# Kernel tuning notes

Hardware: AMD Instinct MI355X
Metric: run time of the kernel (lower is better)

Reference implementation:

```python
import jax, jax.numpy as jnp
import numpy as np

K = 5            # kernel_size per dim
KD = K ** 3      # 125 spline weight slots
DIM = 3
NUM_GRAPHS = 64
# (n_nodes, n_edges, c_in, c_mid, c_out) per pyramid level
LEVELS = [(20000, 320000, 1, 32, 64), (10000, 160000, 1, 64, 64),
          (5000, 80000, 1, 64, 64), (2500, 40000, 1, 64, 64), (1250, 20000, 1, 64, 64)]


def setup_inputs() -> dict:
    key = jax.random.key(0)
    inp = {}
    for i, (n, e, cin, c1, c2) in enumerate(LEVELS, start=1):
        ks = jax.random.split(jax.random.fold_in(key, i), 8)
        inp[f'x{i}'] = jax.random.normal(ks[0], (n, cin), jnp.float32)
        inp[f'pseudo{i}'] = jax.random.uniform(ks[1], (e, DIM), jnp.float32)  # in [0,1)
        inp[f'edge_index{i}'] = jax.random.randint(ks[2], (2, e), 0, n)
        inp[f'batch{i}'] = jnp.sort(jax.random.randint(ks[3], (n,), 0, NUM_GRAPHS))
        inp[f'W{i}a'] = 0.1 * jax.random.normal(ks[4], (KD, cin, c1), jnp.float32)
        inp[f'root{i}a'] = 0.1 * jax.random.normal(ks[5], (cin, c1), jnp.float32)
        inp[f'bias{i}a'] = jnp.zeros((c1,), jnp.float32)
        inp[f'W{i}b'] = 0.1 * jax.random.normal(ks[6], (KD, c1, c2), jnp.float32)
        inp[f'root{i}b'] = 0.1 * jax.random.normal(ks[7], (c1, c2), jnp.float32)
        inp[f'bias{i}b'] = jnp.zeros((c2,), jnp.float32)
    kf = jax.random.fold_in(key, 99)
    inp['fc_w'] = 0.05 * jax.random.normal(kf, (5 * 64, 10), jnp.float32)
    inp['fc_b'] = jnp.zeros((10,), jnp.float32)
    return inp


def _spline_conv(x, src, dst, pseudo, W, Wroot, bias):
    """Degree-1 open B-spline conv (torch_spline_conv), mean aggregation + root weight."""
    n, cin = x.shape
    v = pseudo * (K - 1)                       # [E,3], pseudo in [0,1)
    k0 = jnp.floor(v).astype(jnp.int32)        # lower knot index per dim
    frac = v - k0                              # fractional part per dim
    xs = x[src]                                # [E,cin] gather source feats
    # accumulate basis-weighted source features per (target node, kernel slot)
    acc = jnp.zeros((n, KD, cin), x.dtype)
    for bits in range(2 ** DIM):               # 8 corner combinations of linear spline
        w = jnp.ones((src.shape[0],), x.dtype)
        idx = jnp.zeros((src.shape[0],), jnp.int32)
        for d in range(DIM):
            b = (bits >> d) & 1
            w = w * (frac[:, d] if b else 1.0 - frac[:, d])
            idx = idx * K + (k0[:, d] + b)
        acc = acc.at[dst, idx].add(w[:, None] * xs)
    deg = jnp.zeros((n,), x.dtype).at[dst].add(1.0)
    out = jnp.einsum('nki,kio->no', acc, W) / jnp.maximum(deg, 1.0)[:, None]
    return out + x @ Wroot + bias


def _readout(f, batch):
    s = jax.ops.segment_sum(f, batch, num_segments=NUM_GRAPHS)
    cnt = jax.ops.segment_sum(jnp.ones((f.shape[0],), f.dtype), batch, num_segments=NUM_GRAPHS)
    return s / jnp.maximum(cnt, 1.0)[:, None]   # scatter_mean


def _level(x, ei, ps, bt, Wa, ra, ba, Wb, rb, bb):
    f = jax.nn.relu(_spline_conv(x, ei[0], ei[1], ps, Wa, ra, ba))
    f = jax.nn.relu(_spline_conv(f, ei[0], ei[1], ps, Wb, rb, bb))
    return _readout(f, bt)


def reference(x1, pseudo1, edge_index1, batch1, W1a, root1a, bias1a, W1b, root1b, bias1b,
              x2, pseudo2, edge_index2, batch2, W2a, root2a, bias2a, W2b, root2b, bias2b,
              x3, pseudo3, edge_index3, batch3, W3a, root3a, bias3a, W3b, root3b, bias3b,
              x4, pseudo4, edge_index4, batch4, W4a, root4a, bias4a, W4b, root4b, bias4b,
              x5, pseudo5, edge_index5, batch5, W5a, root5a, bias5a, W5b, root5b, bias5b,
              fc_w, fc_b):
    levels = [
        (x1, edge_index1, pseudo1, batch1, W1a, root1a, bias1a, W1b, root1b, bias1b),
        (x2, edge_index2, pseudo2, batch2, W2a, root2a, bias2a, W2b, root2b, bias2b),
        (x3, edge_index3, pseudo3, batch3, W3a, root3a, bias3a, W3b, root3b, bias3b),
        (x4, edge_index4, pseudo4, batch4, W4a, root4a, bias4a, W4b, root4b, bias4b),
        (x5, edge_index5, pseudo5, batch5, W5a, root5a, bias5a, W5b, root5b, bias5b),
    ]
    res = [_level(*lv) for lv in levels]
    h = jnp.concatenate(res, axis=1)            # [B,320]; eval mode -> dropout is identity
    logits = h @ fc_w + fc_b                    # [B,10]
    return jax.nn.log_softmax(logits, axis=1)
```

## Files before the change

### kernel.cpp

```cpp
#include <hip/hip_runtime.h>
#include <hip/hip_fp16.h>
#include <math.h>

#define NUM_GRAPHS 64

typedef unsigned short ushortT;
typedef __attribute__((ext_vector_type(8))) short bf16x8;
typedef __attribute__((ext_vector_type(4))) float f32x4;

constexpr int cN[5]       = {20000, 10000, 5000, 2500, 1250};
constexpr int cE[5]       = {320000, 160000, 80000, 40000, 20000};
constexpr int cNOFF[6]    = {0, 20000, 30000, 35000, 37500, 38750};
constexpr int cEOFF[6]    = {0, 320000, 480000, 560000, 600000, 620000};
constexpr int cEBLKOFF[6] = {0, 1250, 1875, 2188, 2345, 2424};
constexpr int cNBLKOFF[6] = {0, 79, 119, 139, 149, 154};
constexpr int cMT[5]      = {5064, 2564, 1314, 689, 377};
constexpr int cTILEOFF[6] = {0, 5064, 7628, 8942, 9631, 10008};
constexpr int cSEOFF[6]   = {0, 324096, 488192, 572288, 616384, 640512};
constexpr int cF1OFF[6]   = {0, 640000, 1280000, 1600000, 1760000, 1840000};
constexpr int cWOFF[6]    = {0, 32000, 96000, 160000, 224000, 288000};
constexpr int cABLK[6]    = {0, 1250, 1875, 2188, 2345, 2424};
constexpr int cRBOFF[5]   = {0, 256, 768, 1280, 1792};
constexpr int cWAOFF[6]   = {0, 512, 1536, 2560, 3584, 4608};
constexpr int cRGB[6]     = {0, 313, 470, 549, 589, 609};

struct P5f { const float* p[5]; };
struct P5i { const int* p[5]; };

__device__ __forceinline__ int lvl_e(int b) {
    return (b >= cEBLKOFF[4]) ? 4 : (b >= cEBLKOFF[3]) ? 3 : (b >= cEBLKOFF[2]) ? 2 : (b >= cEBLKOFF[1]) ? 1 : 0;
}
__device__ __forceinline__ int lvl_n(int b) {
    return (b >= cNBLKOFF[4]) ? 4 : (b >= cNBLKOFF[3]) ? 3 : (b >= cNBLKOFF[2]) ? 2 : (b >= cNBLKOFF[1]) ? 1 : 0;
}

__device__ __forceinline__ ushortT f2bf(float f) {
    union { float f; unsigned int u; } v; v.f = f;
    unsigned int r = (v.u + 0x7FFFu + ((v.u >> 16) & 1u)) >> 16;
    return (ushortT)r;
}
__device__ __forceinline__ float h2f_lo(unsigned int u) {
    return __half2float(__ushort_as_half((ushortT)(u & 0xFFFFu)));
}
__device__ __forceinline__ float h2f_hi(unsigned int u) {
    return __half2float(__ushort_as_half((ushortT)(u >> 16)));
}

__global__ void k_hist(P5f PS, P5i EI, int* __restrict__ dcnt, int* __restrict__ bb) {
    int b = blockIdx.x;
    int l = lvl_e(b);
    int lb = b - cEBLKOFF[l];
    int E = cE[l];
    __shared__ int h[64];
    int t = threadIdx.x;
    if (t < 64) h[t] = 0;
    __syncthreads();
    int e = lb * 256 + t;
    if (e < E) {
        atomicAdd(&dcnt[cNOFF[l] + EI.p[l][E + e]], 1);
        const float* ps = PS.p[l];
        int c = (int)floorf(ps[e * 3] * 4.f) * 16 + (int)floorf(ps[e * 3 + 1] * 4.f) * 4
              + (int)floorf(ps[e * 3 + 2] * 4.f);
        atomicAdd(&h[c], 1);
    }
    __syncthreads();
    if (t < 64) bb[(size_t)b * 64 + t] = h[t];
}

__global__ void k_cellscan(int* __restrict__ bb_all, int* __restrict__ csPad,
                           int* __restrict__ cellTot, int* __restrict__ cot_all) {
    int l = blockIdx.x;
    int c = threadIdx.x;
    int* bb = bb_all + (size_t)cEBLKOFF[l] * 64;
    int nblk = cEBLKOFF[l + 1] - cEBLKOFF[l];
    int run = 0;
    int b = 0;
    for (; b + 16 <= nblk; b += 16) {
        int v[16];
#pragma unroll
        for (int u = 0; u < 16; u++) v[u] = bb[(b + u) * 64 + c];
#pragma unroll
        for (int u = 0; u < 16; u++) { bb[(b + u) * 64 + c] = run; run += v[u]; }
    }
    for (; b < nblk; b++) { int v = bb[b * 64 + c]; bb[b * 64 + c] = run; run += v; }
    int tot = run;
    cellTot[l * 64 + c] = tot;
    int tiles = (tot + 63) >> 6;
    int x = tiles;
#pragma unroll
    for (int off = 1; off < 64; off <<= 1) { int y = __shfl_up(x, off, 64); if (c >= off) x += y; }
    int tileBase = x - tiles;
    csPad[l * 64 + c] = tileBase * 64;
    int* cot = cot_all + cTILEOFF[l];
    for (int i = 0; i < tiles; i++) cot[tileBase + i] = c;
    int nT = __shfl(x, 63, 64);
    int mt = cMT[l];
    for (int i = nT + c; i < mt; i += 64) cot[i] = -1;
}

__global__ void k_nscan1(const int* __restrict__ dcnt, int* __restrict__ dbase, int* __restrict__ bsum) {
    int b = blockIdx.x;
    int l = lvl_n(b);
    int lb = b - cNBLKOFF[l];
    int n = cN[l];
    __shared__ int sh[256];
    int t = threadIdx.x;
    int i = lb * 256 + t;
    int v = (i < n) ? dcnt[cNOFF[l] + i] : 0;
    sh[t] = v;
    __syncthreads();
    for (int off = 1; off < 256; off <<= 1) {
        int y = (t >= off) ? sh[t - off] : 0;
        __syncthreads();
        sh[t] += y;
        __syncthreads();
    }
    if (i < n) dbase[cNOFF[l] + i] = sh[t] - v;
    if (t == 255) bsum[b] = sh[255];
}

__global__ void k_nscan2(const int* __restrict__ bsum, int* __restrict__ boff) {
    int l = blockIdx.x;
    int o = cNBLKOFF[l];
    int nb = cNBLKOFF[l + 1] - o;
    int t = threadIdx.x;
    int v = (t < nb) ? bsum[o + t] : 0;
    int s = v;
#pragma unroll
    for (int off = 1; off < 64; off <<= 1) { int y = __shfl_up(s, off, 64); if (t >= off) s += y; }
    int tot = __shfl(s, 63, 64);
    if (t < nb) boff[o + t] = s - v;
    int t2 = t + 64;
    int v2 = (t2 < nb) ? bsum[o + t2] : 0;
    int s2 = v2;
#pragma unroll
    for (int off = 1; off < 64; off <<= 1) { int y = __shfl_up(s2, off, 64); if (t >= off) s2 += y; }
    if (t2 < nb) boff[o + t2] = tot + s2 - v2;
}

__global__ void k_scatter(P5f PS, P5i EI, const int* __restrict__ bb, const int* __restrict__ csPad,
                          const int* __restrict__ dbase, const int* __restrict__ boff,
                          int* __restrict__ rank,
                          int4* __restrict__ cbrec, int4* __restrict__ darec,
                          int* __restrict__ cpos) {
    int b = blockIdx.x;
    int l = lvl_e(b);
    int lb = b - cEBLKOFF[l];
    int E = cE[l];
    __shared__ int base[64];
    __shared__ int cnt[64];
    int t = threadIdx.x;
    if (t < 64) { base[t] = bb[(size_t)b * 64 + t] + csPad[l * 64 + t]; cnt[t] = 0; }
    __syncthreads();
    int e = lb * 256 + t;
    if (e >= E) return;
    const float* ps = PS.p[l];
    float v0 = ps[e * 3] * 4.f, v1 = ps[e * 3 + 1] * 4.f, v2 = ps[e * 3 + 2] * 4.f;
    float f0 = floorf(v0), f1v = floorf(v1), f2v = floorf(v2);
    int c = (int)f0 * 16 + (int)f1v * 4 + (int)f2v;
    int r = atomicAdd(&cnt[c], 1);
    int posc = base[c] + r;
    const int* ei = EI.p[l];
    int src = ei[e];
    int dst = ei[E + e];
    int posd = dbase[cNOFF[l] + dst] + boff[cNBLKOFF[l] + (dst >> 8)]
             + atomicAdd(&rank[cNOFF[l] + dst], 1);
    unsigned int fxfy = (unsigned int)__half_as_ushort(__float2half(v0 - f0))
                      | ((unsigned int)__half_as_ushort(__float2half(v1 - f1v)) << 16);
    unsigned int fzp  = (unsigned int)__half_as_ushort(__float2half(v2 - f2v));
    int4 rc;
    rc.x = src; rc.y = 0; rc.z = (int)fxfy; rc.w = (int)fzp;
    cbrec[cSEOFF[l] + posc] = rc;
    int4 rd;
    rd.x = src | (dst << 16); rd.y = c; rd.z = (int)fxfy; rd.w = (int)fzp;
    darec[cEOFF[l] + posd] = rd;
    cpos[cEOFF[l] + posd] = posc;
}

__global__ void k_wswz(P5f WB, P5f RootB, P5f WA,
                       uint4* __restrict__ hi4, uint4* __restrict__ rb, uint4* __restrict__ wa) {
    int idx = blockIdx.x * 256 + threadIdx.x;
    if (idx >= 294912) return;
    if (idx < 288000) {
        int l = (idx >= 224000) ? 4 : (idx >= 160000) ? 3 : (idx >= 96000) ? 2 : (idx >= 32000) ? 1 : 0;
        int local = idx - cWOFF[l];
        int T = l ? 2 : 1, C = l ? 64 : 32;
        int lane = local & 63;
        int blk = (local >> 6) & 3;
        int rest = local >> 8;
        int st = rest % T, s = rest / T;
        int q = lane >> 4, n = blk * 16 + (lane & 15);
        const float* W = WB.p[l];
        union { ushortT u[8]; uint4 v; } ph;
#pragma unroll
        for (int j = 0; j < 8; j++) {
            int k = st * 32 + q * 8 + j;
            ph.u[j] = f2bf(W[((size_t)s * C + k) * 64 + n]);
        }
        hi4[idx] = ph.v;
    } else if (idx < 290304) {
        int id2 = idx - 288000;
        int l = (id2 >= 1792) ? 4 : (id2 >= 1280) ? 3 : (id2 >= 768) ? 2 : (id2 >= 256) ? 1 : 0;
        int local = id2 - cRBOFF[l];
        int lane = local & 63;
        int w = (local >> 6) & 3;
        int st = local >> 8;
        int q = lane >> 4, n = w * 16 + (lane & 15);
        const float* R = RootB.p[l];
        union { ushortT u[8]; uint4 v; } ph;
#pragma unroll
        for (int j = 0; j < 8; j++) {
            int k = st * 32 + q * 8 + j;
            ph.u[j] = f2bf(R[k * 64 + n]);
        }
        rb[id2] = ph.v;
    } else {
        int id3 = idx - 290304;
        int l = (id3 >= cWAOFF[4]) ? 4 : (id3 >= cWAOFF[3]) ? 3 : (id3 >= cWAOFF[2]) ? 2 : (id3 >= cWAOFF[1]) ? 1 : 0;
        int local = id3 - cWAOFF[l];
        int C1 = l ? 64 : 32;
        int numN = C1 / 16;
        int lane = local & 63;
        int rest = local >> 6;
        int nb = rest % numN, st = rest / numN;
        int q = lane >> 4, n = nb * 16 + (lane & 15);
        const float* Wsrc = WA.p[l];
        union { ushortT u[8]; uint4 v; } ph;
#pragma unroll
        for (int j = 0; j < 8; j++) {
            int k = st * 32 + q * 8 + j;
            ph.u[j] = (k < 125) ? f2bf(Wsrc[k * C1 + n]) : (ushortT)0;
        }
        wa[id3] = ph.v;
    }
}

__launch_bounds__(256)
__global__ void conv_a_fused(P5f X, P5f RootA, P5f BiasA,
                             const int4* __restrict__ darec, const uint4* __restrict__ wasw,
                             const int* __restrict__ dbase, const int* __restrict__ boff,
                             const int* __restrict__ dcnt, ushortT* __restrict__ f1bf) {
    __shared__ float S[16 * 126];
    __shared__ ushortT Sbf[16 * 136];
    __shared__ int infoS[256];
    __shared__ unsigned int fxyS[256];
    __shared__ unsigned int fzS[256];
    __shared__ float xsS[256];
    int b = blockIdx.x;
    int l = (b >= cABLK[4]) ? 4 : (b >= cABLK[3]) ? 3 : (b >= cABLK[2]) ? 2 : (b >= cABLK[1]) ? 1 : 0;
    int node0 = (b - cABLK[l]) * 16;
    int n = cN[l];
    int nn = n - node0; if (nn > 16) nn = 16;
    int t = threadIdx.x;
    for (int i = t; i < 16 * 126; i += 256) S[i] = 0.f;
    const int* db = dbase + cNOFF[l];
    const int* bo = boff + cNBLKOFF[l];
    int estart = db[node0] + bo[node0 >> 8];
    int vend = node0 + nn;
    int eend = (vend >= n) ? cE[l] : (db[vend] + bo[vend >> 8]);
    const float* x = X.p[l];
    const int4* dr = darec + cEOFF[l];
    const int bx = t & 1, by = (t >> 1) & 1, bz = (t >> 2) & 1;
    for (int cs = estart; cs < eend; cs += 256) {
        int p = cs + t;
        if (p < eend) {
            int4 r = dr[p];
            infoS[t] = ((((unsigned int)r.x) >> 16) - node0) * 64 + r.y;
            fxyS[t] = (unsigned int)r.z;
            fzS[t] = (unsigned int)r.w;
            xsS[t] = x[r.x & 0xFFFF];
        }
        __syncthreads();
        int ne = eend - cs; if (ne > 256) ne = 256;
        for (int j = (t >> 3); j < ne; j += 32) {
            int info = infoS[j];
            int nl = info >> 6, cell = info & 63;
            unsigned int uz = fxyS[j];
            float fx = h2f_lo(uz), fy = h2f_hi(uz), fz = h2f_lo(fzS[j]);
            float xs = xsS[j];
            int cx = cell >> 4, cy = (cell >> 2) & 3, cz = cell & 3;
            int slot = (cx + bx) * 25 + (cy + by) * 5 + (cz + bz);
            float wc = (bx ? fx : 1.f - fx) * (by ? fy : 1.f - fy) * (bz ? fz : 1.f - fz);
            atomicAdd(&S[nl * 126 + slot], wc * xs);
        }
        __syncthreads();
    }
    for (int i = t; i < 16 * 128; i += 256) {
        int node = i >> 7, k = i & 127;
        float v = (k < 126) ? S[node * 126 + k] : 0.f;
        Sbf[node * 136 + k] = f2bf(v);
    }
    __syncthreads();
    int lane = t & 63, w = t >> 6;
    int C1 = l ? 64 : 32;
    int numN = C1 >> 4;
    if (w < numN) {
        int q = lane >> 4, m = lane & 15;
        const uint4* wl = wasw + cWAOFF[l];
        f32x4 acc = (f32x4){0.f, 0.f, 0.f, 0.f};
#pragma unroll
        for (int st = 0; st < 4; st++) {
            bf16x8 a = *(const bf16x8*)&Sbf[m * 136 + st * 32 + q * 8];
            bf16x8 bw = __builtin_bit_cast(bf16x8, wl[(st * numN + w) * 64 + lane]);
            acc = __builtin_amdgcn_mfma_f32_16x16x32_bf16(a, bw, acc, 0, 0, 0);
        }
        int ch = w * 16 + m;
        float rv = RootA.p[l][ch], bv = BiasA.p[l][ch];
        const int* dcl = dcnt + cNOFF[l];
        ushortT* f1bfl = f1bf + cF1OFF[l];
#pragma unroll
        for (int rr = 0; rr < 4; rr++) {
            int row = q * 4 + rr;
            if (row < nn) {
                int gnode = node0 + row;
                int dv = dcl[gnode];
                float d = (float)(dv > 1 ? dv : 1);
                float o = acc[rr] / d + x[gnode] * rv + bv;
                f1bfl[(size_t)gnode * C1 + ch] = f2bf(fmaxf(o, 0.f));
            }
        }
    }
}

__launch_bounds__(256)
__global__ void k_rgemm(const ushortT* __restrict__ f1bf, const uint4* __restrict__ rb,
                        float* __restrict__ f2) {
    int b = blockIdx.x;
    int l = (b >= cRGB[4]) ? 4 : (b >= cRGB[3]) ? 3 : (b >= cRGB[2]) ? 2 : (b >= cRGB[1]) ? 1 : 0;
    int node0 = (b - cRGB[l]) * 64;
    int n = cN[l];
    int nn = n - node0; if (nn > 64) nn = 64;
    int t = threadIdx.x;
    int lane = t & 63, w = t >> 6;
    int q = lane >> 4, m = lane & 15;
    const int CIN = l ? 64 : 32;
    const int T = l ? 2 : 1;
    const ushortT* fl = f1bf + cF1OFF[l];
    const uint4* rbl = rb + cRBOFF[l];
    f32x4 C[4];
#pragma unroll
    for (int mt = 0; mt < 4; mt++) C[mt] = (f32x4){0.f, 0.f, 0.f, 0.f};
    for (int st = 0; st < T; st++) {
        bf16x8 bh = __builtin_bit_cast(bf16x8, rbl[(st * 4 + w) * 64 + lane]);
#pragma unroll
        for (int mt = 0; mt < 4; mt++) {
            int row = 16 * mt + m;
            int nr = node0 + row; if (nr > n - 1) nr = n - 1;
            bf16x8 a = *(const bf16x8*)&fl[(size_t)nr * CIN + st * 32 + q * 8];
            C[mt] = __builtin_amdgcn_mfma_f32_16x16x32_bf16(a, bh, C[mt], 0, 0, 0);
        }
    }
#pragma unroll
    for (int mt = 0; mt < 4; mt++)
#pragma unroll
        for (int rr = 0; rr < 4; rr++) {
            int row = 16 * mt + q * 4 + rr;
            if (row < nn)
                f2[(size_t)(cNOFF[l] + node0 + row) * 64 + 16 * w + m] = C[mt][rr];
        }
}

template<int CIN>
__device__ __forceinline__ void conv_b_tile(
    const ushortT* __restrict__ f1bfl, const int4* __restrict__ cbrec_l,
    const uint4* __restrict__ whiL,
    int cell, int tb, int valid, __half* __restrict__ pout,
    float* wxyS , float* fzS , int* srcs) {
    const int T = CIN / 32;
    int t = threadIdx.x;
    if (t < 64) {
        bool v = t < valid;
        int4 r;
        if (v) r = cbrec_l[tb + t]; else { r.x = 0; r.y = 0; r.z = 0; r.w = 0; }
        srcs[t] = r.x;
        unsigned int uz = (unsigned int)r.z;
        float fx = h2f_lo(uz), fy = h2f_hi(uz);
        float gx = 1.f - fx, gy = 1.f - fy;
        wxyS[0 * 64 + t] = gx * gy;
        wxyS[1 * 64 + t] = fx * gy;
        wxyS[2 * 64 + t] = gx * fy;
        wxyS[3 * 64 + t] = fx * fy;
        fzS[t] = h2f_lo((unsigned int)r.w);
    }
    __syncthreads();

    int lane = t & 63, w = t >> 6;
    int q = lane >> 4, m = lane & 15;

    bf16x8 ahr[4][T];
#pragma unroll
    for (int mt = 0; mt < 4; mt++) {
        int src = srcs[16 * mt + m];
#pragma unroll
        for (int st = 0; st < T; st++)
            ahr[mt][st] = *(const bf16x8*)&f1bfl[(size_t)src * CIN + st * 32 + q * 8];
    }
    float fzr[16];
#pragma unroll
    for (int mt = 0; mt < 4; mt++)
#pragma unroll
        for (int rr = 0; rr < 4; rr++)
            fzr[mt * 4 + rr] = fzS[16 * mt + q * 4 + rr];

    int cx = cell >> 4, cy = (cell >> 2) & 3, cz = cell & 3;
    f32x4 acc[4];
#pragma unroll
    for (int mt = 0; mt < 4; mt++) acc[mt] = (f32x4){0.f, 0.f, 0.f, 0.f};

#pragma unroll
    for (int xy = 0; xy < 4; xy++) {
        const int bx = xy & 1, by = xy >> 1;
        int slot0 = (cx + bx) * 25 + (cy + by) * 5 + cz;
        f32x4 C0[4], C1[4];
#pragma unroll
        for (int mt = 0; mt < 4; mt++) {
            C0[mt] = (f32x4){0.f, 0.f, 0.f, 0.f};
            C1[mt] = (f32x4){0.f, 0.f, 0.f, 0.f};
        }
#pragma unroll
        for (int st = 0; st < T; st++) {
            bf16x8 b0 = __builtin_bit_cast(bf16x8, whiL[((size_t)(slot0 * T + st) * 4 + w) * 64 + lane]);
            bf16x8 b1 = __builtin_bit_cast(bf16x8, whiL[((size_t)((slot0 + 1) * T + st) * 4 + w) * 64 + lane]);
#pragma unroll
            for (int mt = 0; mt < 4; mt++) {
                C0[mt] = __builtin_amdgcn_mfma_f32_16x16x32_bf16(ahr[mt][st], b0, C0[mt], 0, 0, 0);
                C1[mt] = __builtin_amdgcn_mfma_f32_16x16x32_bf16(ahr[mt][st], b1, C1[mt], 0, 0, 0);
            }
        }
        const float* wrow = &wxyS[xy * 64];
#pragma unroll
        for (int mt = 0; mt < 4; mt++)
#pragma unroll
            for (int rr = 0; rr < 4; rr++) {
                int i16 = mt * 4 + rr;
                float wxy = wrow[16 * mt + q * 4 + rr];
                float dlt = C1[mt][rr] - C0[mt][rr];
                float tt = fmaf(fzr[i16], dlt, C0[mt][rr]);
                acc[mt][rr] = fmaf(wxy, tt, acc[mt][rr]);
            }
    }
#pragma unroll
    for (int mt = 0; mt < 4; mt++)
#pragma unroll
        for (int rr = 0; rr < 4; rr++) {
            int row = 16 * mt + q * 4 + rr;
            pout[(size_t)(tb + row) * 64 + 16 * w + m] = __float2half(acc[mt][rr]);
        }
}

__launch_bounds__(256)
__global__ void conv_b_all(const ushortT* __restrict__ f1bf, const int4* __restrict__ cbrec,
                           const uint4* __restrict__ whi,
                           const int* __restrict__ cot, const int* __restrict__ csPad,
                           const int* __restrict__ cellTot, __half* __restrict__ Ph) {
    __shared__ float wxyS[4 * 64];
    __shared__ float fzS[64];
    __shared__ int srcs[64];
    int blk = blockIdx.x;
    if (blk < 5064) {
        int cell = cot[blk];
        if (cell < 0) return;
        int tb = blk * 64;
        int valid = csPad[cell] + cellTot[cell] - tb;
        if (valid > 64) valid = 64;
        conv_b_tile<32>(f1bf, cbrec, whi, cell, tb, valid, Ph, wxyS, fzS, srcs);
    } else {
        const int TB2[4] = {0, 2564, 3878, 4567};
        int b2 = blk - 5064;
        int li = (b2 >= 4567) ? 3 : (b2 >= 3878) ? 2 : (b2 >= 2564) ? 1 : 0;
        int l = li + 1;
        int tile = b2 - TB2[li];
        int cell = cot[cTILEOFF[l] + tile];
        if (cell < 0) return;
        int tb = tile * 64;
        int valid = csPad[l * 64 + cell] + cellTot[l * 64 + cell] - tb;
        if (valid > 64) valid = 64;
        conv_b_tile<64>(f1bf + cF1OFF[l], cbrec + cSEOFF[l], whi + cWOFF[l],
                        cell, tb, valid, Ph + (size_t)cSEOFF[l] * 64,
                        wxyS, fzS, srcs);
    }
}

__launch_bounds__(256)
__global__ void node_b_all(const __half* __restrict__ Ph, const int* __restrict__ cpos,
                           const int* __restrict__ dbase, const int* __restrict__ boff,
                           const int* __restrict__ dcnt, P5f BiasB, float* __restrict__ f2) {
    int lane = threadIdx.x & 63;
    int blk = blockIdx.x;
    int l, node;
    if (blk < 5000) {
        l = 0;
        node = blk * 4 + (threadIdx.x >> 6);
        if (node >= 20000) return;
    } else {
        const int NB2[4] = {0, 2500, 3750, 4375};
        int b2 = blk - 5000;
        int li = (b2 >= 4375) ? 3 : (b2 >= 3750) ? 2 : (b2 >= 2500) ? 1 : 0;
        l = li + 1;
        node = (b2 - NB2[li]) * 4 + (threadIdx.x >> 6);
        if (node >= cN[l]) return;
    }
    int start = dbase[cNOFF[l] + node] + boff[cNBLKOFF[l] + (node >> 8)];
    int deg = dcnt[cNOFF[l] + node];
    const __half* PhL = Ph + (size_t)cSEOFF[l] * 64;
    const int* cposL = cpos + cEOFF[l];
    float* f2row = f2 + (size_t)(cNOFF[l] + node) * 64;
    float s0 = 0.f, s1 = 0.f, s2 = 0.f, s3 = 0.f;
    int k = 0;
    for (; k + 4 <= deg; k += 4) {
        int r0 = cposL[start + k];
        int r1 = cposL[start + k + 1];
        int r2 = cposL[start + k + 2];
        int r3 = cposL[start + k + 3];
        s0 += __half2float(PhL[(size_t)r0 * 64 + lane]);
        s1 += __half2float(PhL[(size_t)r1 * 64 + lane]);
        s2 += __half2float(PhL[(size_t)r2 * 64 + lane]);
        s3 += __half2float(PhL[(size_t)r3 * 64 + lane]);
    }
    for (; k < deg; k++) s0 += __half2float(PhL[(size_t)cposL[start + k] * 64 + lane]);
    float s = (s0 + s1) + (s2 + s3);
    s /= (float)(deg > 1 ? deg : 1);
    s += f2row[lane] + BiasB.p[l][lane];
    f2row[lane] = fmaxf(s, 0.f);
}

__launch_bounds__(256)
__global__ void k_read(const float* __restrict__ f2, P5i Batch,
                       float* __restrict__ hsum, float* __restrict__ gcnt) {
    const int RC[5] = {0, 1250, 1875, 2188, 2345};
    int t = threadIdx.x;
    int lane = t & 63;
    int w = blockIdx.x * 4 + (t >> 6);
    if (w >= 2424) return;
    int l = (w >= 2345) ? 4 : (w >= 2188) ? 3 : (w >= 1875) ? 2 : (w >= 1250) ? 1 : 0;
    int base = (w - RC[l]) * 16;
    int Nl = cN[l];
    int nn = Nl - base; if (nn > 16) nn = 16;
    const int* batch = Batch.p[l];
    const float* fb = f2 + (size_t)(cNOFF[l] + base) * 64;
    int curg = -1; float hacc = 0.f; int crun = 0;
    for (int j = 0; j < nn; j++) {
        int g = batch[base + j];
        if (g != curg) {
            if (curg >= 0) {
                atomicAdd(&hsum[curg * 320 + l * 64 + lane], hacc);
                if (lane == 0) atomicAdd(&gcnt[l * 64 + curg], (float)crun);
            }
            curg = g; hacc = 0.f; crun = 0;
        }
        hacc += fb[(size_t)j * 64 + lane];
        crun++;
    }
    if (curg >= 0) {
        atomicAdd(&hsum[curg * 320 + l * 64 + lane], hacc);
        if (lane == 0) atomicAdd(&gcnt[l * 64 + curg], (float)crun);
    }
}

__global__ void fc_kernel(const float* __restrict__ hsum, const float* __restrict__ gcnt,
                          const float* __restrict__ fcw, const float* __restrict__ fcb,
                          float* __restrict__ out) {
    int g = blockIdx.x;
    int lane = threadIdx.x;
    float partial[10];
#pragma unroll
    for (int t = 0; t < 10; t++) partial[t] = 0.f;
#pragma unroll
    for (int k = 0; k < 5; k++) {
        int j = k * 64 + lane;
        float c = fmaxf(gcnt[k * 64 + g], 1.f);
        float h = hsum[g * 320 + j] / c;
        const float* fw = fcw + j * 10;
#pragma unroll
        for (int t = 0; t < 10; t++) partial[t] = fmaf(h, fw[t], partial[t]);
    }
#pragma unroll
    for (int off = 32; off >= 1; off >>= 1)
#pragma unroll
        for (int t = 0; t < 10; t++) partial[t] += __shfl_xor(partial[t], off, 64);
    if (lane == 0) {
        float logit[10];
#pragma unroll
        for (int t = 0; t < 10; t++) logit[t] = partial[t] + fcb[t];
        float m = logit[0];
#pragma unroll
        for (int t = 1; t < 10; t++) m = fmaxf(m, logit[t]);
        float sum = 0.f;
#pragma unroll
        for (int t = 0; t < 10; t++) sum += expf(logit[t] - m);
        float lse = m + logf(sum);
#pragma unroll
        for (int t = 0; t < 10; t++) out[g * 10 + t] = logit[t] - lse;
    }
}

extern "C" void kernel_launch(void* const* d_in, const int* in_sizes, int n_in,
                              void* d_out, int out_size, void* d_ws, size_t ws_size,
                              hipStream_t stream) {
    int* wsI = (int*)d_ws;
    int*   dcnt  = wsI;
    int*   rank  = dcnt + 38750;
    float* hsum  = (float*)(rank + 38750);
    float* gcnt  = hsum + 20480;
    float* f2    = gcnt + 320;
    int*   dbase = (int*)(f2 + 2480000);
    int*   bsum  = dbase + 38750;
    int*   boff  = bsum + 160;
    int*   cpos  = boff + 160;
    int*   bb    = cpos + 620000;
    int*   csPad = bb + 155136;
    int*   cellTot = csPad + 320;
    int*   cot   = cellTot + 320;
    int4*  cbrec = (int4*)(((size_t)(cot + 10008) + 15) & ~(size_t)15);
    int4*  darec = cbrec + 640512;
    ushortT* f1bf = (ushortT*)(darec + 620000);
    uint4* whi   = (uint4*)(((size_t)(f1bf + 1840000) + 15) & ~(size_t)15);
    uint4* rbsw  = whi + 288000;
    uint4* wasw  = rbsw + 2304;
    __half* Ph   = (__half*)(wasw + 4608);

    hipMemsetAsync(dcnt, 0, (size_t)(38750 * 2 + 20480 + 320) * sizeof(int), stream);

    P5f PS, X, WA, RootA, BiasA, WB, RootB, BiasB;
    P5i EI, Batch;
    for (int l = 0; l < 5; l++) {
        const int b = l * 10;
        X.p[l]     = (const float*)d_in[b + 0];
        PS.p[l]    = (const float*)d_in[b + 1];
        EI.p[l]    = (const int*)d_in[b + 2];
        Batch.p[l] = (const int*)d_in[b + 3];
        WA.p[l]    = (const float*)d_in[b + 4];
        RootA.p[l] = (const float*)d_in[b + 5];
        BiasA.p[l] = (const float*)d_in[b + 6];
        WB.p[l]    = (const float*)d_in[b + 7];
        RootB.p[l] = (const float*)d_in[b + 8];
        BiasB.p[l] = (const float*)d_in[b + 9];
    }

    k_hist<<<2424, 256, 0, stream>>>(PS, EI, dcnt, bb);
    k_cellscan<<<5, 64, 0, stream>>>(bb, csPad, cellTot, cot);
    k_nscan1<<<154, 256, 0, stream>>>(dcnt, dbase, bsum);
    k_nscan2<<<5, 64, 0, stream>>>(bsum, boff);
    k_scatter<<<2424, 256, 0, stream>>>(PS, EI, bb, csPad, dbase, boff, rank,
                                        cbrec, darec, cpos);
    k_wswz<<<1152, 256, 0, stream>>>(WB, RootB, WA, whi, rbsw, wasw);

    conv_a_fused<<<2424, 256, 0, stream>>>(X, RootA, BiasA, darec, wasw,
                                           dbase, boff, dcnt, f1bf);

    k_rgemm<<<609, 256, 0, stream>>>(f1bf, rbsw, f2);

    conv_b_all<<<10008, 256, 0, stream>>>(f1bf, cbrec, whi, cot, csPad, cellTot, Ph);
    node_b_all<<<9688, 256, 0, stream>>>(Ph, cpos, dbase, boff, dcnt, BiasB, f2);

    k_read<<<606, 256, 0, stream>>>(f2, Batch, hsum, gcnt);
    fc_kernel<<<64, 64, 0, stream>>>(hsum, gcnt, (const float*)d_in[50], (const float*)d_in[51],
                                     (float*)d_out);
}
```

Before: 454.5 us.

## Make conv_b waves self-contained and double-buffer spline weight loads

Each tile descriptor in cot now also packs the valid-edge count, so conv_b no longer reads csPad or cellTot. Every wave loads its own edge records and shares source indices through __shfl, with a wave barrier in place of the block-wide __syncthreads. Weight fragments for the next xy corner are prefetched into registers while the current corner's MFMAs run, and launch bounds now ask for 3 blocks per SM. The prefetch buffers raise register pressure, and each of the four waves now redundantly loads the same edge records.

```diff
diff --git a/kernel.cpp b/kernel.cpp
--- a/kernel.cpp
+++ b/kernel.cpp
@@ -92,7 +92,10 @@
     int tileBase = x - tiles;
     csPad[l * 64 + c] = tileBase * 64;
     int* cot = cot_all + cTILEOFF[l];
-    for (int i = 0; i < tiles; i++) cot[tileBase + i] = c;
+    for (int i = 0; i < tiles; i++) {
+        int vv = tot - (i << 6); if (vv > 64) vv = 64;
+        cot[tileBase + i] = c | (vv << 8);
+    }
     int nT = __shfl(x, 63, 64);
     int mt = cMT[l];
     for (int i = nT + c; i < mt; i += 64) cot[i] = -1;
@@ -361,36 +364,18 @@
 }
 
 template<int CIN>
-__device__ __forceinline__ void conv_b_tile(
-    const ushortT* __restrict__ f1bfl, const int4* __restrict__ cbrec_l,
-    const uint4* __restrict__ whiL,
-    int cell, int tb, int valid, __half* __restrict__ pout,
-    float* wxyS , float* fzS , int* srcs) {
+__device__ __forceinline__ void conv_b_wave(
+    const ushortT* __restrict__ f1bfl, const uint4* __restrict__ whiL,
+    __half* __restrict__ pout, const float* __restrict__ wxy,
+    const float* __restrict__ fzp, int mySrc, int cell, int tb, int lane, int wv) {
     const int T = CIN / 32;
-    int t = threadIdx.x;
-    if (t < 64) {
-        bool v = t < valid;
-        int4 r;
-        if (v) r = cbrec_l[tb + t]; else { r.x = 0; r.y = 0; r.z = 0; r.w = 0; }
-        srcs[t] = r.x;
-        unsigned int uz = (unsigned int)r.z;
-        float fx = h2f_lo(uz), fy = h2f_hi(uz);
-        float gx = 1.f - fx, gy = 1.f - fy;
-        wxyS[0 * 64 + t] = gx * gy;
-        wxyS[1 * 64 + t] = fx * gy;
-        wxyS[2 * 64 + t] = gx * fy;
-        wxyS[3 * 64 + t] = fx * fy;
-        fzS[t] = h2f_lo((unsigned int)r.w);
-    }
-    __syncthreads();
-
-    int lane = t & 63, w = t >> 6;
     int q = lane >> 4, m = lane & 15;
+    int cx = cell >> 4, cy = (cell >> 2) & 3, cz = cell & 3;
 
     bf16x8 ahr[4][T];
 #pragma unroll
     for (int mt = 0; mt < 4; mt++) {
-        int src = srcs[16 * mt + m];
+        int src = __shfl(mySrc, 16 * mt + m, 64);
 #pragma unroll
         for (int st = 0; st < T; st++)
             ahr[mt][st] = *(const bf16x8*)&f1bfl[(size_t)src * CIN + st * 32 + q * 8];
@@ -400,17 +385,28 @@
     for (int mt = 0; mt < 4; mt++)
 #pragma unroll
         for (int rr = 0; rr < 4; rr++)
-            fzr[mt * 4 + rr] = fzS[16 * mt + q * 4 + rr];
-
-    int cx = cell >> 4, cy = (cell >> 2) & 3, cz = cell & 3;
+            fzr[mt * 4 + rr] = fzp[16 * mt + q * 4 + rr];
+
+    uint4 wb[2][2 * T];
+    auto loadw = [&](int xy, uint4* dst) {
+        int bx = xy & 1, by = xy >> 1;
+        int s0 = (cx + bx) * 25 + (cy + by) * 5 + cz;
+#pragma unroll
+        for (int st = 0; st < T; st++) {
+            dst[st]     = whiL[((size_t)(s0 * T + st) * 4 + wv) * 64 + lane];
+            dst[T + st] = whiL[((size_t)((s0 + 1) * T + st) * 4 + wv) * 64 + lane];
+        }
+    };
+    loadw(0, wb[0]);
+
     f32x4 acc[4];
 #pragma unroll
     for (int mt = 0; mt < 4; mt++) acc[mt] = (f32x4){0.f, 0.f, 0.f, 0.f};
 
 #pragma unroll
     for (int xy = 0; xy < 4; xy++) {
-        const int bx = xy & 1, by = xy >> 1;
-        int slot0 = (cx + bx) * 25 + (cy + by) * 5 + cz;
+        uint4* cur = wb[xy & 1];
+        if (xy < 3) loadw(xy + 1, wb[(xy + 1) & 1]);
         f32x4 C0[4], C1[4];
 #pragma unroll
         for (int mt = 0; mt < 4; mt++) {
@@ -419,24 +415,23 @@
         }
 #pragma unroll
         for (int st = 0; st < T; st++) {
-            bf16x8 b0 = __builtin_bit_cast(bf16x8, whiL[((size_t)(slot0 * T + st) * 4 + w) * 64 + lane]);
-            bf16x8 b1 = __builtin_bit_cast(bf16x8, whiL[((size_t)((slot0 + 1) * T + st) * 4 + w) * 64 + lane]);
+            bf16x8 b0 = __builtin_bit_cast(bf16x8, cur[st]);
+            bf16x8 b1 = __builtin_bit_cast(bf16x8, cur[T + st]);
 #pragma unroll
             for (int mt = 0; mt < 4; mt++) {
                 C0[mt] = __builtin_amdgcn_mfma_f32_16x16x32_bf16(ahr[mt][st], b0, C0[mt], 0, 0, 0);
                 C1[mt] = __builtin_amdgcn_mfma_f32_16x16x32_bf16(ahr[mt][st], b1, C1[mt], 0, 0, 0);
             }
         }
-        const float* wrow = &wxyS[xy * 64];
+        const float* wrow = &wxy[xy * 64];
 #pragma unroll
         for (int mt = 0; mt < 4; mt++)
 #pragma unroll
             for (int rr = 0; rr < 4; rr++) {
-                int i16 = mt * 4 + rr;
-                float wxy = wrow[16 * mt + q * 4 + rr];
+                float wxyv = wrow[16 * mt + q * 4 + rr];
                 float dlt = C1[mt][rr] - C0[mt][rr];
-                float tt = fmaf(fzr[i16], dlt, C0[mt][rr]);
-                acc[mt][rr] = fmaf(wxy, tt, acc[mt][rr]);
+                float tt = fmaf(fzr[mt * 4 + rr], dlt, C0[mt][rr]);
+                acc[mt][rr] = fmaf(wxyv, tt, acc[mt][rr]);
             }
     }
 #pragma unroll
@@ -444,41 +439,44 @@
 #pragma unroll
         for (int rr = 0; rr < 4; rr++) {
             int row = 16 * mt + q * 4 + rr;
-            pout[(size_t)(tb + row) * 64 + 16 * w + m] = __float2half(acc[mt][rr]);
-        }
-}
-
-__launch_bounds__(256)
+            pout[(size_t)(tb + row) * 64 + 16 * wv + m] = __float2half(acc[mt][rr]);
+        }
+}
+
+__launch_bounds__(256, 3)
 __global__ void conv_b_all(const ushortT* __restrict__ f1bf, const int4* __restrict__ cbrec,
-                           const uint4* __restrict__ whi,
-                           const int* __restrict__ cot, const int* __restrict__ csPad,
-                           const int* __restrict__ cellTot, __half* __restrict__ Ph) {
-    __shared__ float wxyS[4 * 64];
-    __shared__ float fzS[64];
-    __shared__ int srcs[64];
-    int blk = blockIdx.x;
-    if (blk < 5064) {
-        int cell = cot[blk];
-        if (cell < 0) return;
-        int tb = blk * 64;
-        int valid = csPad[cell] + cellTot[cell] - tb;
-        if (valid > 64) valid = 64;
-        conv_b_tile<32>(f1bf, cbrec, whi, cell, tb, valid, Ph, wxyS, fzS, srcs);
-    } else {
-        const int TB2[4] = {0, 2564, 3878, 4567};
-        int b2 = blk - 5064;
-        int li = (b2 >= 4567) ? 3 : (b2 >= 3878) ? 2 : (b2 >= 2564) ? 1 : 0;
-        int l = li + 1;
-        int tile = b2 - TB2[li];
-        int cell = cot[cTILEOFF[l] + tile];
-        if (cell < 0) return;
-        int tb = tile * 64;
-        int valid = csPad[l * 64 + cell] + cellTot[l * 64 + cell] - tb;
-        if (valid > 64) valid = 64;
-        conv_b_tile<64>(f1bf + cF1OFF[l], cbrec + cSEOFF[l], whi + cWOFF[l],
-                        cell, tb, valid, Ph + (size_t)cSEOFF[l] * 64,
-                        wxyS, fzS, srcs);
-    }
+                           const uint4* __restrict__ whi, const int* __restrict__ cot,
+                           __half* __restrict__ Ph) {
+    __shared__ float wxyS[4][256];
+    __shared__ float fzS[4][64];
+    int t = threadIdx.x;
+    int wv = t >> 6, lane = t & 63;
+    int ft = blockIdx.x;
+    int l = (ft >= cTILEOFF[4]) ? 4 : (ft >= cTILEOFF[3]) ? 3 : (ft >= cTILEOFF[2]) ? 2 : (ft >= cTILEOFF[1]) ? 1 : 0;
+    int tile = ft - cTILEOFF[l];
+    int desc = cot[ft];
+    int cell  = (desc >= 0) ? (desc & 63) : 0;
+    int valid = (desc >= 0) ? (desc >> 8) : 0;
+    int tb = tile * 64;
+    const int4* cbl = cbrec + cSEOFF[l];
+    int4 r;
+    if (lane < valid) r = cbl[tb + lane];
+    else { r.x = 0; r.y = 0; r.z = 0; r.w = 0; }
+    unsigned int uz = (unsigned int)r.z;
+    float fx = h2f_lo(uz), fy = h2f_hi(uz);
+    float gx = 1.f - fx, gy = 1.f - fy;
+    float* wxy = wxyS[wv];
+    wxy[0 * 64 + lane] = gx * gy;
+    wxy[1 * 64 + lane] = fx * gy;
+    wxy[2 * 64 + lane] = gx * fy;
+    wxy[3 * 64 + lane] = fx * fy;
+    fzS[wv][lane] = h2f_lo((unsigned int)r.w);
+    __builtin_amdgcn_wave_barrier();
+    if (l == 0)
+        conv_b_wave<32>(f1bf, whi, Ph, wxy, fzS[wv], r.x, cell, tb, lane, wv);
+    else
+        conv_b_wave<64>(f1bf + cF1OFF[l], whi + cWOFF[l], Ph + (size_t)cSEOFF[l] * 64,
+                        wxy, fzS[wv], r.x, cell, tb, lane, wv);
 }
 
 __launch_bounds__(256)
@@ -650,7 +648,7 @@
 
     k_rgemm<<<609, 256, 0, stream>>>(f1bf, rbsw, f2);
 
-    conv_b_all<<<10008, 256, 0, stream>>>(f1bf, cbrec, whi, cot, csPad, cellTot, Ph);
+    conv_b_all<<<10008, 256, 0, stream>>>(f1bf, cbrec, whi, cot, Ph);
     node_b_all<<<9688, 256, 0, stream>>>(Ph, cpos, dbase, boff, dcnt, BiasB, f2);
 
     k_read<<<606, 256, 0, stream>>>(f2, Batch, hsum, gcnt);
```

New measurement: 437.4 us. -3.8%, faster.
